# Kernel optimization log

Measured on AMD Instinct MI355X. Metric: run time of the kernel, lower is better.

Reference implementation:

```python
import jax, jax.numpy as jnp
import numpy as np

N = 50000      # nodes
E = 1_600_000  # edges
FN = 8         # num_node_features
FE = 8         # num_edge_features
H = 16         # hidden_layers[0]
IH = 10        # intra_hidden


def _lin(k, i, o):
    return (jax.random.normal(k, (i, o), dtype=jnp.float32) / np.sqrt(i)).astype(jnp.float32)


def setup_inputs() -> dict:
    key = jax.random.key(0)
    ks = jax.random.split(key, 16)
    d = {}
    d["x"] = jax.random.normal(ks[0], (N, FN), dtype=jnp.float32)
    d["edge_attr"] = jax.random.normal(ks[1], (E, FE), dtype=jnp.float32)
    d["edge_index"] = jax.random.randint(ks[2], (2, E), 0, N)
    # NNConv 0: in=FN, out=H; edge-nn: FE -> IH -> FN*H
    d["c0_w1"] = _lin(ks[3], FE, IH);  d["c0_b1"] = jnp.zeros((IH,), jnp.float32)
    d["c0_w2"] = _lin(ks[4], IH, FN * H); d["c0_b2"] = jnp.zeros((FN * H,), jnp.float32)
    d["c0_root"] = _lin(ks[5], FN, H); d["c0_bias"] = jnp.zeros((H,), jnp.float32)
    # NNConv 1: in=H, out=IH; edge-nn: FE -> IH -> H*IH
    d["c1_w1"] = _lin(ks[6], FE, IH);  d["c1_b1"] = jnp.zeros((IH,), jnp.float32)
    d["c1_w2"] = _lin(ks[7], IH, H * IH); d["c1_b2"] = jnp.zeros((H * IH,), jnp.float32)
    d["c1_root"] = _lin(ks[8], H, IH); d["c1_bias"] = jnp.zeros((IH,), jnp.float32)
    # edge predictor: (FE+IH) -> IH -> 1
    d["ep_w1"] = _lin(ks[9], FE + IH, IH); d["ep_b1"] = jnp.zeros((IH,), jnp.float32)
    d["ep_w2"] = _lin(ks[10], IH, 1); d["ep_b2"] = jnp.zeros((1,), jnp.float32)
    return d


def _nnconv(x, edge_index, edge_attr, w1, b1, w2, b2, root, bias, in_ch, out_ch):
    """PyG NNConv (aggr='add', root_weight=True): per-edge weight from edge MLP,
    gather source features, per-edge matvec, scatter-add to targets, plus root term."""
    src, dst = edge_index[0], edge_index[1]
    w = jax.nn.relu(edge_attr @ w1 + b1) @ w2 + b2        # [E, in*out]
    w = w.reshape(-1, in_ch, out_ch)                       # [E, in, out]
    msg = jnp.einsum('ei,eio->eo', x[src], w)              # [E, out]
    agg = jax.ops.segment_sum(msg, dst, num_segments=x.shape[0])  # [N, out]
    return agg + x @ root + bias


def reference(x, edge_attr, edge_index,
              c0_w1, c0_b1, c0_w2, c0_b2, c0_root, c0_bias,
              c1_w1, c1_b1, c1_w2, c1_b2, c1_root, c1_bias,
              ep_w1, ep_b1, ep_w2, ep_b2):
    h = jax.nn.relu(_nnconv(x, edge_index, edge_attr,
                            c0_w1, c0_b1, c0_w2, c0_b2, c0_root, c0_bias, FN, H))
    h = jax.nn.relu(_nnconv(h, edge_index, edge_attr,
                            c1_w1, c1_b1, c1_w2, c1_b2, c1_root, c1_bias, H, IH))
    feat = jnp.concatenate([edge_attr, h[edge_index[0]]], axis=1)  # [E, FE+IH]
    scores = jax.nn.relu(feat @ ep_w1 + ep_b1) @ ep_w2 + ep_b2     # [E, 1]
    return scores.squeeze(-1)
```

## Files before the change

kernel.cpp:

```cpp
#include <hip/hip_runtime.h>

#define N_NODES 50000
#define E_EDGES 1600000
#define FN 8
#define FE 8
#define HID 16
#define IH 10
#define NB_SCAN 196

#define I_OFF   50048
#define I_RANK  100096
#define I_BSUM  1700096
#define I_BBASE 1700352
#define I_TOTAL 1700608
#define F_H     0
#define F_H2    800000
#define F_MSG   1300000
#define F_TOTAL 26900000
#define WS_NEED ((size_t)I_TOTAL*4 + (size_t)F_TOTAL*4)

__global__ __launch_bounds__(256) void count_rank_k(
    const int* __restrict__ ei, int* __restrict__ cntP, int* __restrict__ rank)
{
    int e = blockIdx.x * 256 + threadIdx.x;
    if (e >= E_EDGES) return;
    int dst = ei[E_EDGES + e];
    rank[e] = atomicAdd(&cntP[dst * 16], 1);
}

__global__ __launch_bounds__(256) void blocksum_k(
    const int* __restrict__ cntP, int* __restrict__ bsum)
{
    __shared__ int sh[256];
    int t = threadIdx.x;
    int idx = blockIdx.x * 256 + t;
    sh[t] = (idx < N_NODES) ? cntP[idx * 16] : 0;
    __syncthreads();
#pragma unroll
    for (int d = 128; d > 0; d >>= 1) {
        if (t < d) sh[t] += sh[t + d];
        __syncthreads();
    }
    if (t == 0) bsum[blockIdx.x] = sh[0];
}

__global__ __launch_bounds__(256) void scan_bsums_k(
    const int* __restrict__ bsum, int* __restrict__ bbase)
{
    __shared__ int sh[256];
    int t = threadIdx.x;
    int v = (t < NB_SCAN) ? bsum[t] : 0;
    sh[t] = v;
    __syncthreads();
#pragma unroll
    for (int d = 1; d < 256; d <<= 1) {
        int u = (t >= d) ? sh[t - d] : 0;
        __syncthreads();
        sh[t] += u;
        __syncthreads();
    }
    if (t < NB_SCAN) bbase[t] = sh[t] - v;
}

__global__ __launch_bounds__(256) void offsets_k(
    const int* __restrict__ cntP, const int* __restrict__ bbase,
    int* __restrict__ offset)
{
    __shared__ int sh[256];
    int t = threadIdx.x;
    int b = blockIdx.x;
    int idx = b * 256 + t;
    int v = (idx < N_NODES) ? cntP[idx * 16] : 0;
    sh[t] = v;
    __syncthreads();
#pragma unroll
    for (int d = 1; d < 256; d <<= 1) {
        int u = (t >= d) ? sh[t - d] : 0;
        __syncthreads();
        sh[t] += u;
        __syncthreads();
    }
    int incl = sh[t];
    int base = bbase[b];
    if (idx < N_NODES) offset[idx] = base + incl - v;
    if (idx == N_NODES - 1) offset[N_NODES] = base + incl;
}

__device__ __forceinline__ void load8(const float* __restrict__ p, float v[8]) {
    const float4* q = reinterpret_cast<const float4*>(p);
    float4 a = q[0], b = q[1];
    v[0]=a.x; v[1]=a.y; v[2]=a.z; v[3]=a.w;
    v[4]=b.x; v[5]=b.y; v[6]=b.z; v[7]=b.w;
}

__device__ __forceinline__ void edge_mlp_seq(
    const float eav[FE], const float* __restrict__ w1,
    const float* __restrict__ b1, float u[IH])
{
#pragma unroll
    for (int h = 0; h < IH; ++h) u[h] = b1[h];
#pragma unroll
    for (int k = 0; k < FE; ++k) {
        float ek = eav[k];
#pragma unroll
        for (int h = 0; h < IH; ++h) u[h] = fmaf(ek, w1[k*IH + h], u[h]);
    }
#pragma unroll
    for (int h = 0; h < IH; ++h) u[h] = fmaxf(u[h], 0.f);
}

__device__ __forceinline__ unsigned pk2(float a, float b) {
    unsigned au = __float_as_uint(a) + 0x8000u;
    unsigned bu = __float_as_uint(b) + 0x8000u;
    return (au >> 16) | (bu & 0xFFFF0000u);
}

__device__ __forceinline__ float upbf(unsigned short us) {
    return __uint_as_float(((unsigned)us) << 16);
}

__global__ __launch_bounds__(256) void conv0_scatter_k(
    const float* __restrict__ x, const float* __restrict__ ea,
    const int* __restrict__ ei,
    const float* __restrict__ w1, const float* __restrict__ b1,
    const float* __restrict__ w2, const float* __restrict__ b2,
    const int* __restrict__ offset, const int* __restrict__ rank,
    unsigned* __restrict__ msgu)
{
    __shared__ float smsg[256 * 17];
    __shared__ int   plds[256];

    int t = threadIdx.x;
    int e = blockIdx.x * 256 + t;
    int src = ei[e];
    int dst = ei[E_EDGES + e];
    plds[t] = offset[dst] + rank[e];

    float eav[FE];
    load8(ea + (size_t)e * FE, eav);
    float u[IH];
    edge_mlp_seq(eav, w1, b1, u);
    float xv[FN];
    load8(x + (size_t)src * FN, xv);

    float msg[HID];
#pragma unroll
    for (int o = 0; o < HID; ++o) msg[o] = 0.f;
#pragma unroll
    for (int i = 0; i < FN; ++i) {
        float xi = xv[i];
#pragma unroll
        for (int o = 0; o < HID; ++o)
            msg[o] = fmaf(xi, b2[i*HID + o], msg[o]);
    }
#pragma unroll
    for (int h = 0; h < IH; ++h) {
        float tt[HID];
#pragma unroll
        for (int o = 0; o < HID; ++o) tt[o] = 0.f;
        const float* wp = w2 + h * (FN*HID);
#pragma unroll
        for (int i = 0; i < FN; ++i) {
            float xi = xv[i];
#pragma unroll
            for (int o = 0; o < HID; ++o)
                tt[o] = fmaf(xi, wp[i*HID + o], tt[o]);
        }
        float uh = u[h];
#pragma unroll
        for (int o = 0; o < HID; ++o) msg[o] = fmaf(uh, tt[o], msg[o]);
    }

#pragma unroll
    for (int o = 0; o < HID; ++o) smsg[t*17 + o] = msg[o];
    __syncthreads();

    int q   = t & 1;
    int eb0 = t >> 1;
#pragma unroll
    for (int rep = 0; rep < 2; ++rep) {
        int eL  = eb0 + rep * 128;
        int pos = plds[eL];
        const float* s = &smsg[eL*17 + q*8];
        uint4 v;
        v.x = pk2(s[0], s[1]); v.y = pk2(s[2], s[3]);
        v.z = pk2(s[4], s[5]); v.w = pk2(s[6], s[7]);
        *reinterpret_cast<uint4*>(msgu + (size_t)pos * 8 + q * 4) = v;
    }
}

__global__ __launch_bounds__(256) void node0_red_k(
    const float* __restrict__ x, const unsigned short* __restrict__ msg16,
    const int* __restrict__ offset,
    const float* __restrict__ root, const float* __restrict__ bias,
    float* __restrict__ h)
{
    int idx = blockIdx.x * 256 + threadIdx.x;
    if (idx >= N_NODES * HID) return;
    int n = idx >> 4;
    int o = idx & 15;
    int beg = offset[n], end = offset[n + 1];
    float s = bias[o];
    for (int j = beg; j < end; ++j) s += upbf(msg16[(size_t)j * 16 + o]);
    const float* xr = x + (size_t)n * FN;
#pragma unroll
    for (int i = 0; i < FN; ++i) s = fmaf(xr[i], root[i*HID + o], s);
    h[idx] = fmaxf(s, 0.f);
}

__global__ __launch_bounds__(256) void conv1_scatter_k(
    const float* __restrict__ hin, const float* __restrict__ ea,
    const int* __restrict__ ei,
    const float* __restrict__ w1, const float* __restrict__ b1,
    const float* __restrict__ w2, const float* __restrict__ b2,
    const int* __restrict__ offset, const int* __restrict__ rank,
    unsigned* __restrict__ msgu)
{
    __shared__ float smsg[256 * 17];
    __shared__ int   plds[256];

    int t = threadIdx.x;
    int e = blockIdx.x * 256 + t;
    int src = ei[e];
    int dst = ei[E_EDGES + e];
    plds[t] = offset[dst] + rank[e];

    float eav[FE];
    load8(ea + (size_t)e * FE, eav);
    float u[IH];
    edge_mlp_seq(eav, w1, b1, u);
    float hv[HID];
    load8(hin + (size_t)src * HID,     hv);
    load8(hin + (size_t)src * HID + 8, hv + 8);

    float msg[HID];
#pragma unroll
    for (int o = 0; o < HID; ++o) msg[o] = 0.f;
#pragma unroll
    for (int i = 0; i < HID; ++i) {
        float hi = hv[i];
#pragma unroll
        for (int o = 0; o < IH; ++o)
            msg[o] = fmaf(hi, b2[i*IH + o], msg[o]);
    }
#pragma unroll
    for (int hh = 0; hh < IH; ++hh) {
        float tt[IH];
#pragma unroll
        for (int o = 0; o < IH; ++o) tt[o] = 0.f;
        const float* wp = w2 + hh * (HID*IH);
#pragma unroll
        for (int i = 0; i < HID; ++i) {
            float hi = hv[i];
#pragma unroll
            for (int o = 0; o < IH; ++o)
                tt[o] = fmaf(hi, wp[i*IH + o], tt[o]);
        }
        float uh = u[hh];
#pragma unroll
        for (int o = 0; o < IH; ++o) msg[o] = fmaf(uh, tt[o], msg[o]);
    }

#pragma unroll
    for (int o = 0; o < HID; ++o) smsg[t*17 + o] = msg[o];
    __syncthreads();

    int q   = t & 1;
    int eb0 = t >> 1;
#pragma unroll
    for (int rep = 0; rep < 2; ++rep) {
        int eL  = eb0 + rep * 128;
        int pos = plds[eL];
        const float* s = &smsg[eL*17 + q*8];
        uint4 v;
        v.x = pk2(s[0], s[1]); v.y = pk2(s[2], s[3]);
        v.z = pk2(s[4], s[5]); v.w = pk2(s[6], s[7]);
        *reinterpret_cast<uint4*>(msgu + (size_t)pos * 8 + q * 4) = v;
    }
}

__global__ __launch_bounds__(256) void node1_red_k(
    const float* __restrict__ hin, const unsigned short* __restrict__ msg16,
    const int* __restrict__ offset,
    const float* __restrict__ root, const float* __restrict__ bias,
    float* __restrict__ h2)
{
    int idx = blockIdx.x * 256 + threadIdx.x;
    if (idx >= N_NODES * IH) return;
    int n = idx / IH;
    int o = idx - n * IH;
    int beg = offset[n], end = offset[n + 1];
    float s = bias[o];
    for (int j = beg; j < end; ++j) s += upbf(msg16[(size_t)j * 16 + o]);
    const float* hr = hin + (size_t)n * HID;
#pragma unroll
    for (int i = 0; i < HID; ++i) s = fmaf(hr[i], root[i*IH + o], s);
    h2[idx] = fmaxf(s, 0.f);
}

__global__ __launch_bounds__(256) void edge_pred_k(
    const float* __restrict__ h2, const float* __restrict__ ea,
    const int* __restrict__ ei,
    const float* __restrict__ w1, const float* __restrict__ b1,
    const float* __restrict__ w2, const float* __restrict__ b2,
    float* __restrict__ out)
{
    int e = blockIdx.x * 256 + threadIdx.x;
    if (e >= E_EDGES) return;
    int src = ei[e];
    float eav[FE];
    load8(ea + (size_t)e * FE, eav);
    float hv[IH];
    {
        const float2* p = reinterpret_cast<const float2*>(h2 + (size_t)src * IH);
        float2 a = p[0], b = p[1], c = p[2], d = p[3], f = p[4];
        hv[0]=a.x; hv[1]=a.y; hv[2]=b.x; hv[3]=b.y; hv[4]=c.x;
        hv[5]=c.y; hv[6]=d.x; hv[7]=d.y; hv[8]=f.x; hv[9]=f.y;
    }
    float t[IH];
#pragma unroll
    for (int j = 0; j < IH; ++j) t[j] = b1[j];
#pragma unroll
    for (int k = 0; k < FE; ++k) {
        float ek = eav[k];
#pragma unroll
        for (int j = 0; j < IH; ++j) t[j] = fmaf(ek, w1[k*IH + j], t[j]);
    }
#pragma unroll
    for (int k = 0; k < IH; ++k) {
        float hk = hv[k];
#pragma unroll
        for (int j = 0; j < IH; ++j) t[j] = fmaf(hk, w1[(FE + k)*IH + j], t[j]);
    }
    float score = b2[0];
#pragma unroll
    for (int j = 0; j < IH; ++j)
        score = fmaf(fmaxf(t[j], 0.f), w2[j], score);
    out[e] = score;
}

__global__ __launch_bounds__(256) void conv0_edge_k(
    const float* __restrict__ x, const float* __restrict__ ea,
    const int* __restrict__ ei,
    const float* __restrict__ w1, const float* __restrict__ b1,
    const float* __restrict__ w2, const float* __restrict__ b2,
    float* __restrict__ agg)
{
    int e = blockIdx.x * 256 + threadIdx.x;
    if (e >= E_EDGES) return;
    int src = ei[e];
    int dst = ei[E_EDGES + e];
    float eav[FE];
    load8(ea + (size_t)e * FE, eav);
    float u[IH];
    edge_mlp_seq(eav, w1, b1, u);
    float xv[FN];
    load8(x + (size_t)src * FN, xv);
    float msg[HID];
#pragma unroll
    for (int o = 0; o < HID; ++o) msg[o] = 0.f;
#pragma unroll
    for (int i = 0; i < FN; ++i) {
        float xi = xv[i];
#pragma unroll
        for (int o = 0; o < HID; ++o)
            msg[o] = fmaf(xi, b2[i*HID + o], msg[o]);
    }
#pragma unroll
    for (int h = 0; h < IH; ++h) {
        float t[HID];
#pragma unroll
        for (int o = 0; o < HID; ++o) t[o] = 0.f;
        const float* wp = w2 + h * (FN*HID);
#pragma unroll
        for (int i = 0; i < FN; ++i) {
            float xi = xv[i];
#pragma unroll
            for (int o = 0; o < HID; ++o)
                t[o] = fmaf(xi, wp[i*HID + o], t[o]);
        }
        float uh = u[h];
#pragma unroll
        for (int o = 0; o < HID; ++o) msg[o] = fmaf(uh, t[o], msg[o]);
    }
    float* ap = agg + (size_t)dst * HID;
#pragma unroll
    for (int o = 0; o < HID; ++o) atomicAdd(ap + o, msg[o]);
}

__global__ __launch_bounds__(256) void node0_k(
    const float* __restrict__ x, const float* __restrict__ agg,
    const float* __restrict__ root, const float* __restrict__ bias,
    float* __restrict__ h)
{
    int idx = blockIdx.x * 256 + threadIdx.x;
    if (idx >= N_NODES * HID) return;
    int n = idx >> 4;
    int o = idx & 15;
    float s = agg[idx] + bias[o];
    const float* xr = x + (size_t)n * FN;
#pragma unroll
    for (int i = 0; i < FN; ++i) s = fmaf(xr[i], root[i*HID + o], s);
    h[idx] = fmaxf(s, 0.f);
}

__global__ __launch_bounds__(256) void conv1_edge_k(
    const float* __restrict__ hin, const float* __restrict__ ea,
    const int* __restrict__ ei,
    const float* __restrict__ w1, const float* __restrict__ b1,
    const float* __restrict__ w2, const float* __restrict__ b2,
    float* __restrict__ agg)
{
    int e = blockIdx.x * 256 + threadIdx.x;
    if (e >= E_EDGES) return;
    int src = ei[e];
    int dst = ei[E_EDGES + e];
    float eav[FE];
    load8(ea + (size_t)e * FE, eav);
    float u[IH];
    edge_mlp_seq(eav, w1, b1, u);
    float hv[HID];
    load8(hin + (size_t)src * HID,     hv);
    load8(hin + (size_t)src * HID + 8, hv + 8);
    float msg[IH];
#pragma unroll
    for (int o = 0; o < IH; ++o) msg[o] = 0.f;
#pragma unroll
    for (int i = 0; i < HID; ++i) {
        float hi = hv[i];
#pragma unroll
        for (int o = 0; o < IH; ++o)
            msg[o] = fmaf(hi, b2[i*IH + o], msg[o]);
    }
#pragma unroll
    for (int hh = 0; hh < IH; ++hh) {
        float t[IH];
#pragma unroll
        for (int o = 0; o < IH; ++o) t[o] = 0.f;
        const float* wp = w2 + hh * (HID*IH);
#pragma unroll
        for (int i = 0; i < HID; ++i) {
            float hi = hv[i];
#pragma unroll
            for (int o = 0; o < IH; ++o)
                t[o] = fmaf(hi, wp[i*IH + o], t[o]);
        }
        float uh = u[hh];
#pragma unroll
        for (int o = 0; o < IH; ++o) msg[o] = fmaf(uh, t[o], msg[o]);
    }
    float* ap = agg + (size_t)dst * IH;
#pragma unroll
    for (int o = 0; o < IH; ++o) atomicAdd(ap + o, msg[o]);
}

__global__ __launch_bounds__(256) void node1_k(
    const float* __restrict__ hin, const float* __restrict__ agg,
    const float* __restrict__ root, const float* __restrict__ bias,
    float* __restrict__ h2)
{
    int idx = blockIdx.x * 256 + threadIdx.x;
    if (idx >= N_NODES * IH) return;
    int n = idx / IH;
    int o = idx - n * IH;
    float s = agg[idx] + bias[o];
    const float* hr = hin + (size_t)n * HID;
#pragma unroll
    for (int i = 0; i < HID; ++i) s = fmaf(hr[i], root[i*IH + o], s);
    h2[idx] = fmaxf(s, 0.f);
}

extern "C" void kernel_launch(void* const* d_in, const int* in_sizes, int n_in,
                              void* d_out, int out_size, void* d_ws, size_t ws_size,
                              hipStream_t stream) {
    const float* x       = (const float*)d_in[0];
    const float* ea      = (const float*)d_in[1];
    const int*   ei      = (const int*)  d_in[2];
    const float* c0_w1   = (const float*)d_in[3];
    const float* c0_b1   = (const float*)d_in[4];
    const float* c0_w2   = (const float*)d_in[5];
    const float* c0_b2   = (const float*)d_in[6];
    const float* c0_root = (const float*)d_in[7];
    const float* c0_bias = (const float*)d_in[8];
    const float* c1_w1   = (const float*)d_in[9];
    const float* c1_b1   = (const float*)d_in[10];
    const float* c1_w2   = (const float*)d_in[11];
    const float* c1_b2   = (const float*)d_in[12];
    const float* c1_root = (const float*)d_in[13];
    const float* c1_bias = (const float*)d_in[14];
    const float* ep_w1   = (const float*)d_in[15];
    const float* ep_b1   = (const float*)d_in[16];
    const float* ep_w2   = (const float*)d_in[17];
    const float* ep_b2   = (const float*)d_in[18];
    float* out = (float*)d_out;

    int eb = (E_EDGES + 255) / 256;

    if (ws_size >= WS_NEED) {
        int*   wi     = (int*)d_ws;
        int*   offset = wi + I_OFF;
        int*   rank   = wi + I_RANK;
        int*   bsum   = wi + I_BSUM;
        int*   bbase  = wi + I_BBASE;
        float* wf     = (float*)(wi + I_TOTAL);
        float* h      = wf + F_H;
        float* h2     = wf + F_H2;
        int*            cntP  = (int*)(wf + F_MSG);
        unsigned*       msgu  = (unsigned*)(wf + F_MSG);
        unsigned short* msg16 = (unsigned short*)(wf + F_MSG);

        hipMemsetAsync(cntP, 0, (size_t)N_NODES * 16 * sizeof(int), stream);
        count_rank_k<<<eb, 256, 0, stream>>>(ei, cntP, rank);
        blocksum_k<<<NB_SCAN, 256, 0, stream>>>(cntP, bsum);
        scan_bsums_k<<<1, 256, 0, stream>>>(bsum, bbase);
        offsets_k<<<NB_SCAN, 256, 0, stream>>>(cntP, bbase, offset);

        conv0_scatter_k<<<eb, 256, 0, stream>>>(x, ea, ei, c0_w1, c0_b1, c0_w2, c0_b2,
                                                offset, rank, msgu);
        node0_red_k<<<(N_NODES*HID + 255)/256, 256, 0, stream>>>(x, msg16, offset,
                                                                 c0_root, c0_bias, h);
        conv1_scatter_k<<<eb, 256, 0, stream>>>(h, ea, ei, c1_w1, c1_b1, c1_w2, c1_b2,
                                                offset, rank, msgu);
        node1_red_k<<<(N_NODES*IH + 255)/256, 256, 0, stream>>>(h, msg16, offset,
                                                                c1_root, c1_bias, h2);
        edge_pred_k<<<eb, 256, 0, stream>>>(h2, ea, ei, ep_w1, ep_b1, ep_w2, ep_b2, out);
    } else {
        float* ws   = (float*)d_ws;
        float* agg0 = ws;
        float* agg1 = ws + 800000;
        float* h    = ws + 1300000;
        float* h2   = ws + 2100000;
        hipMemsetAsync(d_ws, 0, 1300000 * sizeof(float), stream);
        conv0_edge_k<<<eb, 256, 0, stream>>>(x, ea, ei, c0_w1, c0_b1, c0_w2, c0_b2, agg0);
        node0_k<<<(N_NODES*HID + 255)/256, 256, 0, stream>>>(x, agg0, c0_root, c0_bias, h);
        conv1_edge_k<<<eb, 256, 0, stream>>>(h, ea, ei, c1_w1, c1_b1, c1_w2, c1_b2, agg1);
        node1_k<<<(N_NODES*IH + 255)/256, 256, 0, stream>>>(h, agg1, c1_root, c1_bias, h2);
        edge_pred_k<<<eb, 256, 0, stream>>>(h2, ea, ei, ep_w1, ep_b1, ep_w2, ep_b2, out);
    }
}
```

Baseline: 279.2 us.

## Precompute per-node x·W2 tables in bf16 to cut per-edge NNConv math

Adds per-node kernels that compute the source features times each hidden slice of the edge-MLP second-layer weights (plus bias term) and store them as a bf16 table. The edge scatter kernels then form messages as a weighted sum of gathered table rows using the edge hidden activations, instead of recomputing the full matvec per edge. This removes most per-edge FMAs but greatly increases the bytes gathered per edge and adds bf16 rounding of intermediate products.

```diff
diff --git a/kernel.cpp b/kernel.cpp
--- a/kernel.cpp
+++ b/kernel.cpp
@@ -16,6 +16,7 @@
 #define F_H     0
 #define F_H2    800000
 #define F_MSG   1300000
+#define F_YTAB  14100000
 #define F_TOTAL 26900000
 #define WS_NEED ((size_t)I_TOTAL*4 + (size_t)F_TOTAL*4)
 
@@ -114,16 +115,93 @@
     unsigned bu = __float_as_uint(b) + 0x8000u;
     return (au >> 16) | (bu & 0xFFFF0000u);
 }
-
+__device__ __forceinline__ float lo16(unsigned v) { return __uint_as_float(v << 16); }
+__device__ __forceinline__ float hi16(unsigned v) { return __uint_as_float(v & 0xFFFF0000u); }
 __device__ __forceinline__ float upbf(unsigned short us) {
     return __uint_as_float(((unsigned)us) << 16);
 }
 
+__global__ __launch_bounds__(256) void ytab0_k(
+    const float* __restrict__ x,
+    const float* __restrict__ w2, const float* __restrict__ b2,
+    unsigned* __restrict__ ytab)
+{
+    __shared__ float ylds[16][177];
+    int t = threadIdx.x;
+    int nl = t >> 4, o = t & 15;
+    int n = blockIdx.x * 16 + nl;
+
+    float xv[FN];
+    load8(x + (size_t)n * FN, xv);
+
+#pragma unroll
+    for (int h = 0; h < IH; ++h) {
+        float s = 0.f;
+#pragma unroll
+        for (int i = 0; i < FN; ++i) s = fmaf(xv[i], w2[h*(FN*HID) + i*HID + o], s);
+        ylds[nl][h*16 + o] = s;
+    }
+    {
+        float s = 0.f;
+#pragma unroll
+        for (int i = 0; i < FN; ++i) s = fmaf(xv[i], b2[i*HID + o], s);
+        ylds[nl][160 + o] = s;
+    }
+    __syncthreads();
+
+    for (int j = t; j < 16 * 88; j += 256) {
+        int nn = j / 88, k = j - nn * 88;
+        int h = k >> 3, op = k & 7;
+        unsigned v = pk2(ylds[nn][h*16 + 2*op], ylds[nn][h*16 + 2*op + 1]);
+        ytab[(size_t)(blockIdx.x * 16 + nn) * 88 + k] = v;
+    }
+}
+
+__global__ __launch_bounds__(256) void ytab1_k(
+    const float* __restrict__ hin,
+    const float* __restrict__ w2, const float* __restrict__ b2,
+    unsigned* __restrict__ ytab)
+{
+    __shared__ float ylds[16][177];
+    int t = threadIdx.x;
+    int nl = t >> 4, o = t & 15;
+    int n = blockIdx.x * 16 + nl;
+
+    float hv[HID];
+    load8(hin + (size_t)n * HID,     hv);
+    load8(hin + (size_t)n * HID + 8, hv + 8);
+
+#pragma unroll
+    for (int h = 0; h < IH; ++h) {
+        float s = 0.f;
+        if (o < IH) {
+#pragma unroll
+            for (int i = 0; i < HID; ++i) s = fmaf(hv[i], w2[h*(HID*IH) + i*IH + o], s);
+        }
+        ylds[nl][h*16 + o] = s;
+    }
+    {
+        float s = 0.f;
+        if (o < IH) {
+#pragma unroll
+            for (int i = 0; i < HID; ++i) s = fmaf(hv[i], b2[i*IH + o], s);
+        }
+        ylds[nl][160 + o] = s;
+    }
+    __syncthreads();
+
+    for (int j = t; j < 16 * 88; j += 256) {
+        int nn = j / 88, k = j - nn * 88;
+        int h = k >> 3, op = k & 7;
+        unsigned v = (op < 5) ? pk2(ylds[nn][h*16 + 2*op], ylds[nn][h*16 + 2*op + 1]) : 0u;
+        ytab[(size_t)(blockIdx.x * 16 + nn) * 88 + k] = v;
+    }
+}
+
 __global__ __launch_bounds__(256) void conv0_scatter_k(
-    const float* __restrict__ x, const float* __restrict__ ea,
-    const int* __restrict__ ei,
+    const float* __restrict__ ea, const int* __restrict__ ei,
     const float* __restrict__ w1, const float* __restrict__ b1,
-    const float* __restrict__ w2, const float* __restrict__ b2,
+    const unsigned* __restrict__ ytab,
     const int* __restrict__ offset, const int* __restrict__ rank,
     unsigned* __restrict__ msgu)
 {
@@ -140,35 +218,29 @@
     load8(ea + (size_t)e * FE, eav);
     float u[IH];
     edge_mlp_seq(eav, w1, b1, u);
-    float xv[FN];
-    load8(x + (size_t)src * FN, xv);
+
+    const uint4* yr = reinterpret_cast<const uint4*>(ytab + (size_t)src * 88);
 
     float msg[HID];
-#pragma unroll
-    for (int o = 0; o < HID; ++o) msg[o] = 0.f;
-#pragma unroll
-    for (int i = 0; i < FN; ++i) {
-        float xi = xv[i];
-#pragma unroll
-        for (int o = 0; o < HID; ++o)
-            msg[o] = fmaf(xi, b2[i*HID + o], msg[o]);
+    {
+        uint4 a = yr[20], b = yr[21];
+        msg[0]=lo16(a.x);  msg[1]=hi16(a.x);  msg[2]=lo16(a.y);  msg[3]=hi16(a.y);
+        msg[4]=lo16(a.z);  msg[5]=hi16(a.z);  msg[6]=lo16(a.w);  msg[7]=hi16(a.w);
+        msg[8]=lo16(b.x);  msg[9]=hi16(b.x);  msg[10]=lo16(b.y); msg[11]=hi16(b.y);
+        msg[12]=lo16(b.z); msg[13]=hi16(b.z); msg[14]=lo16(b.w); msg[15]=hi16(b.w);
     }
 #pragma unroll
     for (int h = 0; h < IH; ++h) {
-        float tt[HID];
-#pragma unroll
-        for (int o = 0; o < HID; ++o) tt[o] = 0.f;
-        const float* wp = w2 + h * (FN*HID);
-#pragma unroll
-        for (int i = 0; i < FN; ++i) {
-            float xi = xv[i];
-#pragma unroll
-            for (int o = 0; o < HID; ++o)
-                tt[o] = fmaf(xi, wp[i*HID + o], tt[o]);
-        }
+        uint4 a = yr[h*2], b = yr[h*2 + 1];
         float uh = u[h];
-#pragma unroll
-        for (int o = 0; o < HID; ++o) msg[o] = fmaf(uh, tt[o], msg[o]);
+        msg[0]  = fmaf(uh, lo16(a.x), msg[0]);   msg[1]  = fmaf(uh, hi16(a.x), msg[1]);
+        msg[2]  = fmaf(uh, lo16(a.y), msg[2]);   msg[3]  = fmaf(uh, hi16(a.y), msg[3]);
+        msg[4]  = fmaf(uh, lo16(a.z), msg[4]);   msg[5]  = fmaf(uh, hi16(a.z), msg[5]);
+        msg[6]  = fmaf(uh, lo16(a.w), msg[6]);   msg[7]  = fmaf(uh, hi16(a.w), msg[7]);
+        msg[8]  = fmaf(uh, lo16(b.x), msg[8]);   msg[9]  = fmaf(uh, hi16(b.x), msg[9]);
+        msg[10] = fmaf(uh, lo16(b.y), msg[10]);  msg[11] = fmaf(uh, hi16(b.y), msg[11]);
+        msg[12] = fmaf(uh, lo16(b.z), msg[12]);  msg[13] = fmaf(uh, hi16(b.z), msg[13]);
+        msg[14] = fmaf(uh, lo16(b.w), msg[14]);  msg[15] = fmaf(uh, hi16(b.w), msg[15]);
     }
 
 #pragma unroll
@@ -189,6 +261,69 @@
     }
 }
 
+__global__ __launch_bounds__(256) void conv1_scatter_k(
+    const float* __restrict__ ea, const int* __restrict__ ei,
+    const float* __restrict__ w1, const float* __restrict__ b1,
+    const unsigned* __restrict__ ytab,
+    const int* __restrict__ offset, const int* __restrict__ rank,
+    unsigned* __restrict__ msgu)
+{
+    __shared__ float smsg[256 * 17];
+    __shared__ int   plds[256];
+
+    int t = threadIdx.x;
+    int e = blockIdx.x * 256 + t;
+    int src = ei[e];
+    int dst = ei[E_EDGES + e];
+    plds[t] = offset[dst] + rank[e];
+
+    float eav[FE];
+    load8(ea + (size_t)e * FE, eav);
+    float u[IH];
+    edge_mlp_seq(eav, w1, b1, u);
+
+    const unsigned* yr = ytab + (size_t)src * 88;
+
+    float msg[HID];
+    {
+        uint4 a = *reinterpret_cast<const uint4*>(yr + 80);
+        uint2 c = *reinterpret_cast<const uint2*>(yr + 84);
+        msg[0]=lo16(a.x); msg[1]=hi16(a.x); msg[2]=lo16(a.y); msg[3]=hi16(a.y);
+        msg[4]=lo16(a.z); msg[5]=hi16(a.z); msg[6]=lo16(a.w); msg[7]=hi16(a.w);
+        msg[8]=lo16(c.x); msg[9]=hi16(c.x);
+    }
+#pragma unroll
+    for (int h = 0; h < IH; ++h) {
+        uint4 a = *reinterpret_cast<const uint4*>(yr + h*8);
+        uint2 c = *reinterpret_cast<const uint2*>(yr + h*8 + 4);
+        float uh = u[h];
+        msg[0] = fmaf(uh, lo16(a.x), msg[0]);  msg[1] = fmaf(uh, hi16(a.x), msg[1]);
+        msg[2] = fmaf(uh, lo16(a.y), msg[2]);  msg[3] = fmaf(uh, hi16(a.y), msg[3]);
+        msg[4] = fmaf(uh, lo16(a.z), msg[4]);  msg[5] = fmaf(uh, hi16(a.z), msg[5]);
+        msg[6] = fmaf(uh, lo16(a.w), msg[6]);  msg[7] = fmaf(uh, hi16(a.w), msg[7]);
+        msg[8] = fmaf(uh, lo16(c.x), msg[8]);  msg[9] = fmaf(uh, hi16(c.x), msg[9]);
+    }
+#pragma unroll
+    for (int o = IH; o < HID; ++o) msg[o] = 0.f;
+
+#pragma unroll
+    for (int o = 0; o < HID; ++o) smsg[t*17 + o] = msg[o];
+    __syncthreads();
+
+    int q   = t & 1;
+    int eb0 = t >> 1;
+#pragma unroll
+    for (int rep = 0; rep < 2; ++rep) {
+        int eL  = eb0 + rep * 128;
+        int pos = plds[eL];
+        const float* s = &smsg[eL*17 + q*8];
+        uint4 v;
+        v.x = pk2(s[0], s[1]); v.y = pk2(s[2], s[3]);
+        v.z = pk2(s[4], s[5]); v.w = pk2(s[6], s[7]);
+        *reinterpret_cast<uint4*>(msgu + (size_t)pos * 8 + q * 4) = v;
+    }
+}
+
 __global__ __launch_bounds__(256) void node0_red_k(
     const float* __restrict__ x, const unsigned short* __restrict__ msg16,
     const int* __restrict__ offset,
@@ -206,77 +341,6 @@
 #pragma unroll
     for (int i = 0; i < FN; ++i) s = fmaf(xr[i], root[i*HID + o], s);
     h[idx] = fmaxf(s, 0.f);
-}
-
-__global__ __launch_bounds__(256) void conv1_scatter_k(
-    const float* __restrict__ hin, const float* __restrict__ ea,
-    const int* __restrict__ ei,
-    const float* __restrict__ w1, const float* __restrict__ b1,
-    const float* __restrict__ w2, const float* __restrict__ b2,
-    const int* __restrict__ offset, const int* __restrict__ rank,
-    unsigned* __restrict__ msgu)
-{
-    __shared__ float smsg[256 * 17];
-    __shared__ int   plds[256];
-
-    int t = threadIdx.x;
-    int e = blockIdx.x * 256 + t;
-    int src = ei[e];
-    int dst = ei[E_EDGES + e];
-    plds[t] = offset[dst] + rank[e];
-
-    float eav[FE];
-    load8(ea + (size_t)e * FE, eav);
-    float u[IH];
-    edge_mlp_seq(eav, w1, b1, u);
-    float hv[HID];
-    load8(hin + (size_t)src * HID,     hv);
-    load8(hin + (size_t)src * HID + 8, hv + 8);
-
-    float msg[HID];
-#pragma unroll
-    for (int o = 0; o < HID; ++o) msg[o] = 0.f;
-#pragma unroll
-    for (int i = 0; i < HID; ++i) {
-        float hi = hv[i];
-#pragma unroll
-        for (int o = 0; o < IH; ++o)
-            msg[o] = fmaf(hi, b2[i*IH + o], msg[o]);
-    }
-#pragma unroll
-    for (int hh = 0; hh < IH; ++hh) {
-        float tt[IH];
-#pragma unroll
-        for (int o = 0; o < IH; ++o) tt[o] = 0.f;
-        const float* wp = w2 + hh * (HID*IH);
-#pragma unroll
-        for (int i = 0; i < HID; ++i) {
-            float hi = hv[i];
-#pragma unroll
-            for (int o = 0; o < IH; ++o)
-                tt[o] = fmaf(hi, wp[i*IH + o], tt[o]);
-        }
-        float uh = u[hh];
-#pragma unroll
-        for (int o = 0; o < IH; ++o) msg[o] = fmaf(uh, tt[o], msg[o]);
-    }
-
-#pragma unroll
-    for (int o = 0; o < HID; ++o) smsg[t*17 + o] = msg[o];
-    __syncthreads();
-
-    int q   = t & 1;
-    int eb0 = t >> 1;
-#pragma unroll
-    for (int rep = 0; rep < 2; ++rep) {
-        int eL  = eb0 + rep * 128;
-        int pos = plds[eL];
-        const float* s = &smsg[eL*17 + q*8];
-        uint4 v;
-        v.x = pk2(s[0], s[1]); v.y = pk2(s[2], s[3]);
-        v.z = pk2(s[4], s[5]); v.w = pk2(s[6], s[7]);
-        *reinterpret_cast<uint4*>(msgu + (size_t)pos * 8 + q * 4) = v;
-    }
 }
 
 __global__ __launch_bounds__(256) void node1_red_k(
@@ -495,6 +559,7 @@
     float* out = (float*)d_out;
 
     int eb = (E_EDGES + 255) / 256;
+    int nb16 = N_NODES / 16;
 
     if (ws_size >= WS_NEED) {
         int*   wi     = (int*)d_ws;
@@ -508,6 +573,7 @@
         int*            cntP  = (int*)(wf + F_MSG);
         unsigned*       msgu  = (unsigned*)(wf + F_MSG);
         unsigned short* msg16 = (unsigned short*)(wf + F_MSG);
+        unsigned*       ytab  = (unsigned*)(wf + F_YTAB);
 
         hipMemsetAsync(cntP, 0, (size_t)N_NODES * 16 * sizeof(int), stream);
         count_rank_k<<<eb, 256, 0, stream>>>(ei, cntP, rank);
@@ -515,11 +581,13 @@
         scan_bsums_k<<<1, 256, 0, stream>>>(bsum, bbase);
         offsets_k<<<NB_SCAN, 256, 0, stream>>>(cntP, bbase, offset);
 
-        conv0_scatter_k<<<eb, 256, 0, stream>>>(x, ea, ei, c0_w1, c0_b1, c0_w2, c0_b2,
+        ytab0_k<<<nb16, 256, 0, stream>>>(x, c0_w2, c0_b2, ytab);
+        conv0_scatter_k<<<eb, 256, 0, stream>>>(ea, ei, c0_w1, c0_b1, ytab,
                                                 offset, rank, msgu);
         node0_red_k<<<(N_NODES*HID + 255)/256, 256, 0, stream>>>(x, msg16, offset,
                                                                  c0_root, c0_bias, h);
-        conv1_scatter_k<<<eb, 256, 0, stream>>>(h, ea, ei, c1_w1, c1_b1, c1_w2, c1_b2,
+        ytab1_k<<<nb16, 256, 0, stream>>>(h, c1_w2, c1_b2, ytab);
+        conv1_scatter_k<<<eb, 256, 0, stream>>>(ea, ei, c1_w1, c1_b1, ytab,
                                                 offset, rank, msgu);
         node1_red_k<<<(N_NODES*IH + 255)/256, 256, 0, stream>>>(h, msg16, offset,
                                                                 c1_root, c1_bias, h2);
```

New measurement: 413.2 us. 48.0% more time.
